# Kernel optimization log

Hardware: AMD Instinct MI355X
Metric: run time of the kernel (lower is better)

Reference implementation:

```python
import jax, jax.numpy as jnp
import numpy as np

B, IN_DIM, EMB, D_NUM, M_NUM, TAU = 32768, 768, 768, 9, 10, 32.0


def setup_inputs() -> dict:
    key = jax.random.key(0)
    k1, k2, k3, k4, k5 = jax.random.split(key, 5)
    feature = jax.random.normal(k1, (B, IN_DIM), dtype=jnp.float32)
    category = jax.random.randint(k2, (B,), 0, D_NUM, dtype=jnp.int64)
    # nn.Linear(input_dim, emb_dim, bias=False) weights: [emb_dim, input_dim]
    s = 1.0 / np.sqrt(IN_DIM)
    W_topic = jax.random.uniform(k3, (EMB, IN_DIM), jnp.float32, -s, s)
    W_domain = jax.random.uniform(k4, (EMB, IN_DIM), jnp.float32, -s, s)
    # stacked per-domain memory banks: [domain_num, memory_num, emb_dim]
    domain_memory = jax.random.normal(k5, (D_NUM, M_NUM, EMB), dtype=jnp.float32)
    return {"feature": feature, "category": category, "W_topic": W_topic,
            "W_domain": W_domain, "domain_memory": domain_memory}


def reference(feature, category, W_topic, W_domain, domain_memory):
    # norm(x): L2-normalize each row
    length = jnp.sqrt(jnp.sum(feature * feature, axis=1, keepdims=True))
    feature = feature / length
    q_topic = feature @ W_topic.T   # [B, EMB]
    q_dom = feature @ W_domain.T    # [B, EMB]
    # per-domain attention over memory bank, batched over domains
    scores = jnp.einsum('be,dme->bdm', q_topic, domain_memory) * TAU
    topic_att = jax.nn.softmax(scores, axis=-1)                 # [B, D, M]
    sep_emb = jnp.einsum('bdm,dme->bde', topic_att, domain_memory)  # [B, D, EMB]
    domain_att = jnp.einsum('bde,be->bd', sep_emb, q_dom) * TAU
    domain_att = jax.nn.softmax(domain_att, axis=1)[:, None, :]  # [B, 1, D]
    return domain_att
```

## Files before the change

### kernel.cpp

```cpp
#include <hip/hip_runtime.h>
#include <hip/hip_fp8.h>
#include <math.h>

#define TAU 32.0f
#define LO_SCALE 2048.0f
#define INV_LO_SCALE (1.0f/2048.0f)

typedef _Float16 f16x8 __attribute__((ext_vector_type(8)));
typedef float    f32x16 __attribute__((ext_vector_type(16)));

#if defined(__has_builtin)
#if __has_builtin(__builtin_amdgcn_cvt_f32_fp8) && __has_builtin(__builtin_amdgcn_cvt_pk_fp8_f32)
#define HAVE_FP8_BUILTINS 1
#endif
#endif

static __device__ __forceinline__ unsigned char enc_e4m3(float x) {
#ifdef HAVE_FP8_BUILTINS
    int p = __builtin_amdgcn_cvt_pk_fp8_f32(x, x, 0, false);
    return (unsigned char)(p & 0xff);
#else
    __hip_fp8_e4m3 q(x);
    return (unsigned char)q.__x;
#endif
}

#ifdef HAVE_FP8_BUILTINS
#define DEC_E4M3(W, SEL) __builtin_amdgcn_cvt_f32_fp8((int)(W), (SEL))
#else
static __device__ __forceinline__ float dec_e4m3_sw(unsigned w, int sel) {
    __hip_fp8_e4m3 q; q.__x = (unsigned char)((w >> (8 * sel)) & 0xff);
    return (float)q;
}
#define DEC_E4M3(W, SEL) dec_e4m3_sw((W), (SEL))
#endif

__global__ __launch_bounds__(1024) void precompute_mw_packed(
    const float* __restrict__ Wt, const float* __restrict__ Wd,
    const float* __restrict__ dmem, _Float16* __restrict__ PBhi,
    unsigned char* __restrict__ PBlo)
{
    __shared__ float Ml[3 * 768];
    __shared__ float red[3][4][256];
    const int nt  = blockIdx.x;
    const int kc  = blockIdx.y;
    const int n0  = nt * 3;
    const int tid = threadIdx.x;
    const int q   = tid >> 8;
    const int kl  = tid & 255;
    const int k   = kc * 256 + kl;
    float v[3] = {0.f, 0.f, 0.f};
    if (n0 < 180) {
        const float* __restrict__ W = (n0 < 90) ? Wt : Wd;
        const int m0 = (n0 < 90) ? n0 : n0 - 90;
        for (int idx = tid; idx < 3 * 768; idx += 1024)
            Ml[idx] = dmem[m0 * 768 + idx];
        __syncthreads();

        const float* __restrict__ Wq  = W + (q * 192) * 768 + k;
        const float* __restrict__ mlb = Ml + q * 192;
        float a0 = 0.f, a1 = 0.f, a2 = 0.f;
        for (int e0 = 0; e0 < 192; e0 += 8) {
            float w[8];
            #pragma unroll
            for (int i = 0; i < 8; ++i)
                w[i] = Wq[(e0 + i) * 768];
            float4 m0a = *(const float4*)(mlb + e0);
            float4 m0b = *(const float4*)(mlb + e0 + 4);
            float4 m1a = *(const float4*)(mlb + 768 + e0);
            float4 m1b = *(const float4*)(mlb + 768 + e0 + 4);
            float4 m2a = *(const float4*)(mlb + 1536 + e0);
            float4 m2b = *(const float4*)(mlb + 1536 + e0 + 4);
            a0 = fmaf(m0a.x, w[0], a0); a0 = fmaf(m0a.y, w[1], a0);
            a0 = fmaf(m0a.z, w[2], a0); a0 = fmaf(m0a.w, w[3], a0);
            a0 = fmaf(m0b.x, w[4], a0); a0 = fmaf(m0b.y, w[5], a0);
            a0 = fmaf(m0b.z, w[6], a0); a0 = fmaf(m0b.w, w[7], a0);
            a1 = fmaf(m1a.x, w[0], a1); a1 = fmaf(m1a.y, w[1], a1);
            a1 = fmaf(m1a.z, w[2], a1); a1 = fmaf(m1a.w, w[3], a1);
            a1 = fmaf(m1b.x, w[4], a1); a1 = fmaf(m1b.y, w[5], a1);
            a1 = fmaf(m1b.z, w[6], a1); a1 = fmaf(m1b.w, w[7], a1);
            a2 = fmaf(m2a.x, w[0], a2); a2 = fmaf(m2a.y, w[1], a2);
            a2 = fmaf(m2a.z, w[2], a2); a2 = fmaf(m2a.w, w[3], a2);
            a2 = fmaf(m2b.x, w[4], a2); a2 = fmaf(m2b.y, w[5], a2);
            a2 = fmaf(m2b.z, w[6], a2); a2 = fmaf(m2b.w, w[7], a2);
        }
        red[0][q][kl] = a0;
        red[1][q][kl] = a1;
        red[2][q][kl] = a2;
        __syncthreads();
        if (q == 0) {
            #pragma unroll
            for (int i = 0; i < 3; ++i)
                v[i] = red[i][0][kl] + red[i][1][kl] + red[i][2][kl] + red[i][3][kl];
        }
    }
    if (q == 0) {
        const int t = k >> 5, ks = (k >> 4) & 1, h = (k >> 3) & 1, j = k & 7;
        const int fragc = (t * 2 + ks) * 6;
        #pragma unroll
        for (int i = 0; i < 3; ++i) {
            const int n = n0 + i;
            const int idx = (fragc + (n >> 5)) * 512 + (h * 32 + (n & 31)) * 8 + j;
            _Float16 hi = (_Float16)v[i];
            float lo = (v[i] - (float)hi) * LO_SCALE;
            PBhi[idx] = hi;
            PBlo[idx] = enc_e4m3(lo);
        }
    }
}

#define MFMA_BODY(KS, BH, BL) do {                                          \
    const int _ao = (arow * 64 + (KS) * 32 + asel) ^ swzA;                  \
    f16x8 _ah = *(const f16x8*)((const char*)AhL + _ao);                    \
    f16x8 _al = *(const f16x8*)((const char*)AlL + _ao);                    \
    _Pragma("unroll")                                                       \
    for (int _nt = 0; _nt < 3; ++_nt) {                                     \
        f16x8 _bl;                                                          \
        _bl[0] = (_Float16)DEC_E4M3(BL[_nt].x, 0);                          \
        _bl[1] = (_Float16)DEC_E4M3(BL[_nt].x, 1);                          \
        _bl[2] = (_Float16)DEC_E4M3(BL[_nt].x, 2);                          \
        _bl[3] = (_Float16)DEC_E4M3(BL[_nt].x, 3);                          \
        _bl[4] = (_Float16)DEC_E4M3(BL[_nt].y, 0);                          \
        _bl[5] = (_Float16)DEC_E4M3(BL[_nt].y, 1);                          \
        _bl[6] = (_Float16)DEC_E4M3(BL[_nt].y, 2);                          \
        _bl[7] = (_Float16)DEC_E4M3(BL[_nt].y, 3);                          \
        acc1[_nt] = __builtin_amdgcn_mfma_f32_32x32x16_f16(_ah, BH[_nt], acc1[_nt], 0, 0, 0); \
        acc2[_nt] = __builtin_amdgcn_mfma_f32_32x32x16_f16(_ah, _bl,     acc2[_nt], 0, 0, 0); \
        acc2[_nt] = __builtin_amdgcn_mfma_f32_32x32x16_f16(_al, BH[_nt], acc2[_nt], 0, 0, 0); \
    }                                                                       \
} while (0)

__global__ __launch_bounds__(256, 1) void fused_memnet(
    const float* __restrict__ F, const _Float16* __restrict__ PBhi,
    const unsigned char* __restrict__ PBlo, float* __restrict__ out)
{
    __shared__ alignas(16) _Float16 AhL[64 * 32];
    __shared__ alignas(16) _Float16 AlL[64 * 32];
    __shared__ float raw[64 * 196];
    __shared__ float ss[64];

    const int tid  = threadIdx.x;
    const int lane = tid & 63;
    const int wid  = tid >> 6;
    const int wrow = (wid >> 1) * 32;
    const int wcol = (wid & 1) * 96;
    const int row0 = blockIdx.x * 64;

    const int srow = tid >> 2;
    const int sc   = tid & 3;
    const float* __restrict__ Fp = F + (row0 + srow) * 768 + sc * 8;
    const int wb = (srow * 64 + sc * 16) ^ ((srow & 7) << 4);

    const _Float16*      __restrict__ pbh = PBhi + (wid & 1) * 3 * 512 + lane * 8;
    const unsigned char* __restrict__ pbl = PBlo + (wid & 1) * 3 * 512 + lane * 8;

    const int arow = wrow + (lane & 31);
    const int swzA = (arow & 7) << 4;
    const int asel = (lane >> 5) * 16;

    f32x16 acc1[3], acc2[3];
    #pragma unroll
    for (int nt = 0; nt < 3; ++nt)
        #pragma unroll
        for (int r = 0; r < 16; ++r) { acc1[nt][r] = 0.f; acc2[nt][r] = 0.f; }

    float ps = 0.f;
    float4 p0 = *(const float4*)(Fp);
    float4 p1 = *(const float4*)(Fp + 4);

    f16x8 Bh0[3], Bh1[3];
    uint2 Bl0[3], Bl1[3];
    #pragma unroll
    for (int nt = 0; nt < 3; ++nt) {
        Bh0[nt] = *(const f16x8*)(pbh + nt * 512);
        Bl0[nt] = *(const uint2*)(pbl + nt * 512);
    }

    for (int t = 0; t < 24; ++t) {
        __syncthreads();
        {
            f16x8 h8, l8;
            float xs[8] = {p0.x, p0.y, p0.z, p0.w, p1.x, p1.y, p1.z, p1.w};
            #pragma unroll
            for (int i = 0; i < 8; ++i) {
                float x = xs[i];
                _Float16 hh = (_Float16)x;
                h8[i] = hh;
                l8[i] = (_Float16)((x - (float)hh) * LO_SCALE);
                ps += x * x;
            }
            *(f16x8*)((char*)AhL + wb) = h8;
            *(f16x8*)((char*)AlL + wb) = l8;
        }
        if (t < 23) {
            p0 = *(const float4*)(Fp + (t + 1) * 32);
            p1 = *(const float4*)(Fp + (t + 1) * 32 + 4);
        }
        __syncthreads();

        #pragma unroll
        for (int nt = 0; nt < 3; ++nt) {
            Bh1[nt] = *(const f16x8*)(pbh + (2 * t + 1) * 3072 + nt * 512);
            Bl1[nt] = *(const uint2*)(pbl + (2 * t + 1) * 3072 + nt * 512);
        }
        MFMA_BODY(0, Bh0, Bl0);
        if (t < 23) {
            #pragma unroll
            for (int nt = 0; nt < 3; ++nt) {
                Bh0[nt] = *(const f16x8*)(pbh + (2 * t + 2) * 3072 + nt * 512);
                Bl0[nt] = *(const uint2*)(pbl + (2 * t + 2) * 3072 + nt * 512);
            }
        }
        MFMA_BODY(1, Bh1, Bl1);
    }

    ps += __shfl_xor(ps, 1);
    ps += __shfl_xor(ps, 2);
    if (sc == 0) ss[srow] = ps;

    #pragma unroll
    for (int nt = 0; nt < 3; ++nt) {
        const int cl = wcol + nt * 32 + (lane & 31);
        #pragma unroll
        for (int r = 0; r < 16; ++r) {
            const int rl = wrow + (r & 3) + 8 * (r >> 2) + 4 * (lane >> 5);
            raw[rl * 196 + cl] = acc1[nt][r] + acc2[nt][r] * INV_LO_SCALE;
        }
    }
    __syncthreads();

    if (tid < 64) {
        const int r = tid;
        const float s = TAU / sqrtf(ss[r]);
        const float* Sr = raw + r * 196;
        float logit[9];
        #pragma unroll
        for (int d = 0; d < 9; ++d) {
            float vv[10];
            float mx = -1e30f;
            #pragma unroll
            for (int m = 0; m < 10; ++m) {
                vv[m] = s * Sr[d * 10 + m];
                mx = fmaxf(mx, vv[m]);
            }
            float den = 0.f, num = 0.f;
            #pragma unroll
            for (int m = 0; m < 10; ++m) {
                const float e = expf(vv[m] - mx);
                den += e;
                num = fmaf(e, Sr[90 + d * 10 + m], num);
            }
            logit[d] = s * num / den;
        }
        float mx2 = -1e30f;
        #pragma unroll
        for (int d = 0; d < 9; ++d) mx2 = fmaxf(mx2, logit[d]);
        float e2[9], den2 = 0.f;
        #pragma unroll
        for (int d = 0; d < 9; ++d) { e2[d] = expf(logit[d] - mx2); den2 += e2[d]; }
        const float inv = 1.f / den2;
        float* op = out + (row0 + r) * 9;
        #pragma unroll
        for (int d = 0; d < 9; ++d) op[d] = e2[d] * inv;
    }
}

extern "C" void kernel_launch(void* const* d_in, const int* in_sizes, int n_in,
                              void* d_out, int out_size, void* d_ws, size_t ws_size,
                              hipStream_t stream)
{
    const float* feature = (const float*)d_in[0];
    const float* Wt   = (const float*)d_in[2];
    const float* Wd   = (const float*)d_in[3];
    const float* dmem = (const float*)d_in[4];
    float* outp = (float*)d_out;
    _Float16* PBhi = (_Float16*)d_ws;
    unsigned char* PBlo = (unsigned char*)d_ws + 192 * 768 * 2;

    precompute_mw_packed<<<dim3(64, 3), 1024, 0, stream>>>(Wt, Wd, dmem, PBhi, PBlo);
    fused_memnet<<<32768 / 64, 256, 0, stream>>>(feature, PBhi, PBlo, outp);
}
```

Before: 59.88 us.

## Restructure fused kernel to 32-row tiles, 6 waves, double-buffered LDS, packed fp8 decode

Halves the row tile to 32 rows per block and uses six waves, each owning one 32-column N tile instead of three. This should raise occupancy (launch bounds of 6 blocks) and cut accumulator registers. Double-buffers the A tiles in LDS so the fp32-to-split-fp16 conversion of the next K slice overlaps MFMA work, with one barrier per half-step. Switches the fp8 low-part decode to packed conversion builtins. The trade-off is re-reading the packed weight matrix from cache twice as often and leaving two waves idle during A staging.

```diff
diff --git a/kernel.cpp b/kernel.cpp
--- a/kernel.cpp
+++ b/kernel.cpp
@@ -7,11 +7,17 @@
 #define INV_LO_SCALE (1.0f/2048.0f)
 
 typedef _Float16 f16x8 __attribute__((ext_vector_type(8)));
+typedef _Float16 f16x4 __attribute__((ext_vector_type(4)));
+typedef __fp16   fp16v2 __attribute__((ext_vector_type(2)));
+typedef float    f32x2 __attribute__((ext_vector_type(2)));
 typedef float    f32x16 __attribute__((ext_vector_type(16)));
 
 #if defined(__has_builtin)
 #if __has_builtin(__builtin_amdgcn_cvt_f32_fp8) && __has_builtin(__builtin_amdgcn_cvt_pk_fp8_f32)
 #define HAVE_FP8_BUILTINS 1
+#endif
+#if __has_builtin(__builtin_amdgcn_cvt_pk_f32_fp8) && __has_builtin(__builtin_amdgcn_cvt_pkrtz)
+#define HAVE_FP8_PK 1
 #endif
 #endif
 
@@ -34,6 +40,30 @@
 }
 #define DEC_E4M3(W, SEL) dec_e4m3_sw((W), (SEL))
 #endif
+
+static __device__ __forceinline__ f16x8 dec8(uint2 w) {
+    f16x8 r;
+#ifdef HAVE_FP8_PK
+    f32x2 a = __builtin_amdgcn_cvt_pk_f32_fp8((int)w.x, false);
+    f32x2 b = __builtin_amdgcn_cvt_pk_f32_fp8((int)w.x, true);
+    f32x2 c = __builtin_amdgcn_cvt_pk_f32_fp8((int)w.y, false);
+    f32x2 d = __builtin_amdgcn_cvt_pk_f32_fp8((int)w.y, true);
+    fp16v2 h0 = __builtin_amdgcn_cvt_pkrtz(a[0], a[1]);
+    fp16v2 h1 = __builtin_amdgcn_cvt_pkrtz(b[0], b[1]);
+    fp16v2 h2 = __builtin_amdgcn_cvt_pkrtz(c[0], c[1]);
+    fp16v2 h3 = __builtin_amdgcn_cvt_pkrtz(d[0], d[1]);
+    r[0] = (_Float16)h0[0]; r[1] = (_Float16)h0[1];
+    r[2] = (_Float16)h1[0]; r[3] = (_Float16)h1[1];
+    r[4] = (_Float16)h2[0]; r[5] = (_Float16)h2[1];
+    r[6] = (_Float16)h3[0]; r[7] = (_Float16)h3[1];
+#else
+    r[0] = (_Float16)DEC_E4M3(w.x, 0); r[1] = (_Float16)DEC_E4M3(w.x, 1);
+    r[2] = (_Float16)DEC_E4M3(w.x, 2); r[3] = (_Float16)DEC_E4M3(w.x, 3);
+    r[4] = (_Float16)DEC_E4M3(w.y, 0); r[5] = (_Float16)DEC_E4M3(w.y, 1);
+    r[6] = (_Float16)DEC_E4M3(w.y, 2); r[7] = (_Float16)DEC_E4M3(w.y, 3);
+#endif
+    return r;
+}
 
 __global__ __launch_bounds__(1024) void precompute_mw_packed(
     const float* __restrict__ Wt, const float* __restrict__ Wd,
@@ -56,7 +86,6 @@
         for (int idx = tid; idx < 3 * 768; idx += 1024)
             Ml[idx] = dmem[m0 * 768 + idx];
         __syncthreads();
-
         const float* __restrict__ Wq  = W + (q * 192) * 768 + k;
         const float* __restrict__ mlb = Ml + q * 192;
         float a0 = 0.f, a1 = 0.f, a2 = 0.f;
@@ -109,127 +138,110 @@
     }
 }
 
-#define MFMA_BODY(KS, BH, BL) do {                                          \
-    const int _ao = (arow * 64 + (KS) * 32 + asel) ^ swzA;                  \
-    f16x8 _ah = *(const f16x8*)((const char*)AhL + _ao);                    \
-    f16x8 _al = *(const f16x8*)((const char*)AlL + _ao);                    \
-    _Pragma("unroll")                                                       \
-    for (int _nt = 0; _nt < 3; ++_nt) {                                     \
-        f16x8 _bl;                                                          \
-        _bl[0] = (_Float16)DEC_E4M3(BL[_nt].x, 0);                          \
-        _bl[1] = (_Float16)DEC_E4M3(BL[_nt].x, 1);                          \
-        _bl[2] = (_Float16)DEC_E4M3(BL[_nt].x, 2);                          \
-        _bl[3] = (_Float16)DEC_E4M3(BL[_nt].x, 3);                          \
-        _bl[4] = (_Float16)DEC_E4M3(BL[_nt].y, 0);                          \
-        _bl[5] = (_Float16)DEC_E4M3(BL[_nt].y, 1);                          \
-        _bl[6] = (_Float16)DEC_E4M3(BL[_nt].y, 2);                          \
-        _bl[7] = (_Float16)DEC_E4M3(BL[_nt].y, 3);                          \
-        acc1[_nt] = __builtin_amdgcn_mfma_f32_32x32x16_f16(_ah, BH[_nt], acc1[_nt], 0, 0, 0); \
-        acc2[_nt] = __builtin_amdgcn_mfma_f32_32x32x16_f16(_ah, _bl,     acc2[_nt], 0, 0, 0); \
-        acc2[_nt] = __builtin_amdgcn_mfma_f32_32x32x16_f16(_al, BH[_nt], acc2[_nt], 0, 0, 0); \
-    }                                                                       \
+#define LOADB2(S, KL) do {                                   \
+    Bh##S = *(const f16x8*)(pbh + (KL) * 3072);              \
+    Bl##S = *(const uint2*)(pbl + (KL) * 3072);              \
 } while (0)
 
-__global__ __launch_bounds__(256, 1) void fused_memnet(
+#define CONV4(P, BUF) do {                                   \
+    float _xs[4] = {(P).x, (P).y, (P).z, (P).w};             \
+    f16x4 _h, _l;                                            \
+    _Pragma("unroll")                                        \
+    for (int _i = 0; _i < 4; ++_i) {                         \
+        float _x = _xs[_i];                                  \
+        _Float16 _hh = (_Float16)_x;                         \
+        _h[_i] = _hh;                                        \
+        _l[_i] = (_Float16)((_x - (float)_hh) * LO_SCALE);   \
+        ps += _x * _x;                                       \
+    }                                                        \
+    *(f16x4*)((char*)AhL[BUF] + wb) = _h;                    \
+    *(f16x4*)((char*)AlL[BUF] + wb) = _l;                    \
+} while (0)
+
+#define MBODY(BUF, KS, BH, BL) do {                          \
+    const int _ao = (arow * 64 + (KS) * 32 + asel) ^ swzA;   \
+    f16x8 _ah = *(const f16x8*)((const char*)AhL[BUF] + _ao);\
+    f16x8 _al = *(const f16x8*)((const char*)AlL[BUF] + _ao);\
+    f16x8 _bl = dec8(BL);                                    \
+    acc1 = __builtin_amdgcn_mfma_f32_32x32x16_f16(_ah, BH, acc1, 0, 0, 0);  \
+    acc2 = __builtin_amdgcn_mfma_f32_32x32x16_f16(_ah, _bl, acc2, 0, 0, 0); \
+    acc2 = __builtin_amdgcn_mfma_f32_32x32x16_f16(_al, BH, acc2, 0, 0, 0);  \
+} while (0)
+
+__global__ __launch_bounds__(384, 6) void fused_memnet(
     const float* __restrict__ F, const _Float16* __restrict__ PBhi,
     const unsigned char* __restrict__ PBlo, float* __restrict__ out)
 {
-    __shared__ alignas(16) _Float16 AhL[64 * 32];
-    __shared__ alignas(16) _Float16 AlL[64 * 32];
-    __shared__ float raw[64 * 196];
-    __shared__ float ss[64];
+    __shared__ alignas(16) _Float16 AhL[2][32 * 32];
+    __shared__ alignas(16) _Float16 AlL[2][32 * 32];
+    __shared__ float raw[32 * 196];
+    __shared__ float ss[32];
 
     const int tid  = threadIdx.x;
     const int lane = tid & 63;
-    const int wid  = tid >> 6;
-    const int wrow = (wid >> 1) * 32;
-    const int wcol = (wid & 1) * 96;
-    const int row0 = blockIdx.x * 64;
-
-    const int srow = tid >> 2;
-    const int sc   = tid & 3;
-    const float* __restrict__ Fp = F + (row0 + srow) * 768 + sc * 8;
-    const int wb = (srow * 64 + sc * 16) ^ ((srow & 7) << 4);
-
-    const _Float16*      __restrict__ pbh = PBhi + (wid & 1) * 3 * 512 + lane * 8;
-    const unsigned char* __restrict__ pbl = PBlo + (wid & 1) * 3 * 512 + lane * 8;
-
-    const int arow = wrow + (lane & 31);
+    const int wid  = tid / 64;
+    const int row0 = blockIdx.x * 32;
+
+    const int srow = (tid >> 3) & 31;
+    const int sc4  = tid & 7;
+    const float* __restrict__ Fp = F + (row0 + srow) * 768 + sc4 * 4;
+    const int wb = (srow * 64 + sc4 * 8) ^ ((srow & 7) << 4);
+
+    const _Float16*      __restrict__ pbh = PBhi + wid * 512 + lane * 8;
+    const unsigned char* __restrict__ pbl = PBlo + wid * 512 + lane * 8;
+
+    const int arow = lane & 31;
     const int swzA = (arow & 7) << 4;
     const int asel = (lane >> 5) * 16;
 
-    f32x16 acc1[3], acc2[3];
+    f32x16 acc1, acc2;
     #pragma unroll
-    for (int nt = 0; nt < 3; ++nt)
-        #pragma unroll
-        for (int r = 0; r < 16; ++r) { acc1[nt][r] = 0.f; acc2[nt][r] = 0.f; }
+    for (int r = 0; r < 16; ++r) { acc1[r] = 0.f; acc2[r] = 0.f; }
 
     float ps = 0.f;
-    float4 p0 = *(const float4*)(Fp);
-    float4 p1 = *(const float4*)(Fp + 4);
-
-    f16x8 Bh0[3], Bh1[3];
-    uint2 Bl0[3], Bl1[3];
+    float4 p00, ppA, ppB;
+    f16x8 Bh0, Bh1, Bh2, Bh3;
+    uint2 Bl0, Bl1, Bl2, Bl3;
+
+    if (tid < 256) {
+        p00 = *(const float4*)(Fp);
+        ppA = *(const float4*)(Fp + 32);
+        ppB = *(const float4*)(Fp + 64);
+        CONV4(p00, 0);
+    }
+    LOADB2(0, 0);
+    LOADB2(1, 1);
+    __syncthreads();
+
+    for (int th = 0; th < 24; th += 2) {
+        if (th < 23) { LOADB2(2, 2 * th + 2); LOADB2(3, 2 * th + 3); }
+        MBODY(0, 0, Bh0, Bl0);
+        if (tid < 256 && th < 23) CONV4(ppA, 1);
+        if (tid < 256 && th < 21) ppA = *(const float4*)(Fp + (th + 3) * 32);
+        MBODY(0, 1, Bh1, Bl1);
+        __syncthreads();
+        const int T1 = th + 1;
+        if (T1 < 23) { LOADB2(0, 2 * T1 + 2); LOADB2(1, 2 * T1 + 3); }
+        MBODY(1, 0, Bh2, Bl2);
+        if (tid < 256 && T1 < 23) CONV4(ppB, 0);
+        if (tid < 256 && T1 < 21) ppB = *(const float4*)(Fp + (T1 + 3) * 32);
+        MBODY(1, 1, Bh3, Bl3);
+        __syncthreads();
+    }
+
+    if (tid < 256) {
+        ps += __shfl_xor(ps, 1); ps += __shfl_xor(ps, 2); ps += __shfl_xor(ps, 4);
+        if (sc4 == 0) ss[srow] = ps;
+    }
+
     #pragma unroll
-    for (int nt = 0; nt < 3; ++nt) {
-        Bh0[nt] = *(const f16x8*)(pbh + nt * 512);
-        Bl0[nt] = *(const uint2*)(pbl + nt * 512);
-    }
-
-    for (int t = 0; t < 24; ++t) {
-        __syncthreads();
-        {
-            f16x8 h8, l8;
-            float xs[8] = {p0.x, p0.y, p0.z, p0.w, p1.x, p1.y, p1.z, p1.w};
-            #pragma unroll
-            for (int i = 0; i < 8; ++i) {
-                float x = xs[i];
-                _Float16 hh = (_Float16)x;
-                h8[i] = hh;
-                l8[i] = (_Float16)((x - (float)hh) * LO_SCALE);
-                ps += x * x;
-            }
-            *(f16x8*)((char*)AhL + wb) = h8;
-            *(f16x8*)((char*)AlL + wb) = l8;
-        }
-        if (t < 23) {
-            p0 = *(const float4*)(Fp + (t + 1) * 32);
-            p1 = *(const float4*)(Fp + (t + 1) * 32 + 4);
-        }
-        __syncthreads();
-
-        #pragma unroll
-        for (int nt = 0; nt < 3; ++nt) {
-            Bh1[nt] = *(const f16x8*)(pbh + (2 * t + 1) * 3072 + nt * 512);
-            Bl1[nt] = *(const uint2*)(pbl + (2 * t + 1) * 3072 + nt * 512);
-        }
-        MFMA_BODY(0, Bh0, Bl0);
-        if (t < 23) {
-            #pragma unroll
-            for (int nt = 0; nt < 3; ++nt) {
-                Bh0[nt] = *(const f16x8*)(pbh + (2 * t + 2) * 3072 + nt * 512);
-                Bl0[nt] = *(const uint2*)(pbl + (2 * t + 2) * 3072 + nt * 512);
-            }
-        }
-        MFMA_BODY(1, Bh1, Bl1);
-    }
-
-    ps += __shfl_xor(ps, 1);
-    ps += __shfl_xor(ps, 2);
-    if (sc == 0) ss[srow] = ps;
-
-    #pragma unroll
-    for (int nt = 0; nt < 3; ++nt) {
-        const int cl = wcol + nt * 32 + (lane & 31);
-        #pragma unroll
-        for (int r = 0; r < 16; ++r) {
-            const int rl = wrow + (r & 3) + 8 * (r >> 2) + 4 * (lane >> 5);
-            raw[rl * 196 + cl] = acc1[nt][r] + acc2[nt][r] * INV_LO_SCALE;
-        }
+    for (int r = 0; r < 16; ++r) {
+        const int rl = (r & 3) + 8 * (r >> 2) + 4 * (lane >> 5);
+        raw[rl * 196 + wid * 32 + (lane & 31)] = acc1[r] + acc2[r] * INV_LO_SCALE;
     }
     __syncthreads();
 
-    if (tid < 64) {
+    if (tid < 32) {
         const int r = tid;
         const float s = TAU / sqrtf(ss[r]);
         const float* Sr = raw + r * 196;
@@ -278,5 +290,5 @@
     unsigned char* PBlo = (unsigned char*)d_ws + 192 * 768 * 2;
 
     precompute_mw_packed<<<dim3(64, 3), 1024, 0, stream>>>(Wt, Wd, dmem, PBhi, PBlo);
-    fused_memnet<<<32768 / 64, 256, 0, stream>>>(feature, PBhi, PBlo, outp);
-}
+    fused_memnet<<<32768 / 32, 384, 0, stream>>>(feature, PBhi, PBlo, outp);
+}
```

Result: slower. 125.6 us (+109.7%).
